# Optimization experiments

Hardware: AMD Instinct MI355X
Metric: run time of the kernel (lower is better)

## Reference

```python
import jax, jax.numpy as jnp
import numpy as np

HEADS = 16
DIM_HEAD = 64


def setup_inputs() -> dict:
    key = jax.random.key(0)
    k1, k2, k3 = jax.random.split(key, 3)
    b, n, dim = 8, 4096, 1024
    inner = HEADS * DIM_HEAD  # 1024
    x = jax.random.normal(k1, (b, n, dim), dtype=jnp.float32)
    # torch Linear stored transposed; here W_qkv is [in, out] so y = x @ W_qkv
    W_qkv = jax.random.normal(k2, (dim, 4 * inner), dtype=jnp.float32) * (dim ** -0.5)
    W_out = jax.random.normal(k3, (inner, dim), dtype=jnp.float32) * (inner ** -0.5)
    b_out = jnp.zeros((dim,), dtype=jnp.float32)
    return {"x": x, "W_qkv": W_qkv, "W_out": W_out, "b_out": b_out}


def reference(x, W_qkv, W_out, b_out):
    b, n, dim = x.shape
    h, d = HEADS, DIM_HEAD
    scale = d ** -0.5
    qkv = x @ W_qkv  # [b, n, 4*h*d]
    q, k, v, v2 = jnp.split(qkv, 4, axis=-1)
    # rearrange 'b n (h d) -> b h n d'
    to_heads = lambda t: t.reshape(b, n, h, d).transpose(0, 2, 1, 3)
    q, k, v, v2 = map(to_heads, (q, k, v, v2))
    # channel-wise attention: dots = q^T @ k over the sequence axis -> [b,h,d,d]
    dots = jnp.einsum('bhnd,bhne->bhde', q, k) * scale
    attn = jax.nn.softmax(dots, axis=-1)
    # v^T @ v2 -> [b,h,d,d]
    vv = jnp.einsum('bhnd,bhne->bhde', v, v2)
    out = jnp.einsum('bhde,bhef->bhdf', attn, vv)  # [b,h,d,d]
    # rearrange 'b h n d -> b n (h d)' with n == dim_head here
    out = out.transpose(0, 2, 1, 3).reshape(b, d, h * d)  # [b, dim_head, inner]
    return out @ W_out + b_out  # [b, dim_head, dim]
```

## Files before the change

### kernel.cpp

```cpp
#include <hip/hip_runtime.h>
#include <hip/hip_bf16.h>
#include <stdint.h>

typedef _Float16 f16;
typedef _Float16 f16x8 __attribute__((ext_vector_type(8)));
typedef float f32x4 __attribute__((ext_vector_type(4)));

#define AS1 __attribute__((address_space(1)))
#define AS3 __attribute__((address_space(3)))

__global__ __launch_bounds__(256) void tr_cvt_kernel(
    const float* __restrict__ src, f16* __restrict__ dst, int R, int C)
{
    __shared__ float tile[64][65];
    const int b = blockIdx.z;
    src += (size_t)b * R * C;
    dst += (size_t)b * R * C;
    const int c0 = blockIdx.x * 64;
    const int r0 = blockIdx.y * 64;
    const int t = threadIdx.x;
    {
        const int cc = (t & 15) * 4;
        const int rr = t >> 4;
#pragma unroll
        for (int p = 0; p < 4; ++p) {
            const int r = rr + p * 16;
            const float4 v = *(const float4*)(src + (size_t)(r0 + r) * C + c0 + cc);
            tile[r][cc + 0] = v.x; tile[r][cc + 1] = v.y;
            tile[r][cc + 2] = v.z; tile[r][cc + 3] = v.w;
        }
    }
    __syncthreads();
    {
        const int rq = (t & 15) * 4;
        const int cp = t >> 4;
#pragma unroll
        for (int p = 0; p < 4; ++p) {
            const int c = cp + p * 16;
            ushort4 o;
            f16 h0 = (f16)tile[rq + 0][c];
            f16 h1 = (f16)tile[rq + 1][c];
            f16 h2 = (f16)tile[rq + 2][c];
            f16 h3 = (f16)tile[rq + 3][c];
            o.x = __builtin_bit_cast(unsigned short, h0);
            o.y = __builtin_bit_cast(unsigned short, h1);
            o.z = __builtin_bit_cast(unsigned short, h2);
            o.w = __builtin_bit_cast(unsigned short, h3);
            *(ushort4*)(dst + (size_t)(c0 + c) * R + r0 + rq) = o;
        }
    }
}

__device__ __forceinline__ void stage256(
    const f16* __restrict__ src, int ld, char* ldsbase, int tid)
{
    const int lane = tid & 63;
    const int gch = ((lane & 7) ^ (lane >> 3)) * 8;
    const int rowl = tid >> 3;
    const int wbase = (tid >> 3) & ~7;
#pragma unroll
    for (int p = 0; p < 4; ++p) {
        const f16* s = src + (size_t)(p * 64 + rowl) * ld + gch;
        __builtin_amdgcn_global_load_lds(
            (const AS1 uint32_t*)s,
            (AS3 uint32_t*)(ldsbase + (p * 64 + wbase) * 128), 16, 0, 0);
    }
}

__device__ __forceinline__ void gemm256_core(
    const f16* __restrict__ A, const f16* __restrict__ Bt,
    int lda, int ldb, int nsteps,
    f16* As, f16* Bs, f32x4 (&acc)[8][4], int tid)
{
    const int lane = tid & 63, w = tid >> 6;
    const int wr = w >> 2, wc = w & 3;
    const int cl = lane & 15, kg = lane >> 4, b7 = lane & 7;

    stage256(A, lda, (char*)As, tid);
    stage256(Bt, ldb, (char*)Bs, tid);

#pragma unroll 1
    for (int t = 0; t < nsteps; ++t) {
        const int cur = t & 1;
        if (t + 1 < nsteps) {
            const int k0 = (t + 1) * 64;
            stage256(A + k0, lda, (char*)As + (cur ^ 1) * 32768, tid);
            stage256(Bt + k0, ldb, (char*)Bs + (cur ^ 1) * 32768, tid);
            asm volatile("s_waitcnt vmcnt(8)" ::: "memory");
        } else {
            asm volatile("s_waitcnt vmcnt(0)" ::: "memory");
        }
        __builtin_amdgcn_s_barrier();
        const f16* Ab = As + cur * 16384;
        const f16* Bb = Bs + cur * 16384;
#pragma unroll
        for (int kk = 0; kk < 2; ++kk) {
            const int ch = (kk * 4 + kg) ^ b7;
            f16x8 af[8], bf[4];
#pragma unroll
            for (int i = 0; i < 8; ++i)
                af[i] = *(const f16x8*)&Ab[(wr * 128 + i * 16 + cl) * 64 + ch * 8];
#pragma unroll
            for (int j = 0; j < 4; ++j)
                bf[j] = *(const f16x8*)&Bb[(wc * 64 + j * 16 + cl) * 64 + ch * 8];
#pragma unroll
            for (int i = 0; i < 8; ++i)
#pragma unroll
                for (int j = 0; j < 4; ++j)
                    acc[i][j] = __builtin_amdgcn_mfma_f32_16x16x32_f16(af[i], bf[j], acc[i][j], 0, 0, 0);
        }
        __builtin_amdgcn_s_barrier();
    }
}

__global__ __launch_bounds__(512, 2) void gemm_syk256(
    const f16* __restrict__ xT, f16* __restrict__ Gp)
{
    __shared__ f16 As[2 * 256 * 64];
    __shared__ f16 Bs[2 * 256 * 64];
    const int orig = blockIdx.x;
    const int l = (orig & 7) * 32 + (orig >> 3);
    const int tile = l & 15, b = (l >> 4) & 7, s = l >> 7;
    const int ti = tile >> 2, tj = tile & 3;

    const f16* base = xT + (size_t)b * (1024 * 4096) + (size_t)s * 2048;
    const f16* A  = base + (size_t)ti * 256 * 4096;
    const f16* Bt = base + (size_t)tj * 256 * 4096;

    f32x4 acc[8][4];
#pragma unroll
    for (int i = 0; i < 8; ++i)
#pragma unroll
        for (int j = 0; j < 4; ++j) acc[i][j] = f32x4{0.f, 0.f, 0.f, 0.f};

    gemm256_core(A, Bt, 4096, 4096, 32, As, Bs, acc, threadIdx.x);

    f16* out = Gp + ((size_t)s * 8 + b) * 1048576;
    const int lane = threadIdx.x & 63, w = threadIdx.x >> 6;
    const int wr = w >> 2, wc = w & 3;
    const int cl = lane & 15, rg = lane >> 4;
#pragma unroll
    for (int i = 0; i < 8; ++i)
#pragma unroll
        for (int j = 0; j < 4; ++j)
#pragma unroll
            for (int q = 0; q < 4; ++q) {
                const int row = ti * 256 + wr * 128 + i * 16 + rg * 4 + q;
                const int col = tj * 256 + wc * 64 + j * 16 + cl;
                out[(size_t)row * 1024 + col] = (f16)acc[i][j][q];
            }
}

__global__ __launch_bounds__(256) void reduce_sum(
    const f16* __restrict__ Gp, f16* __restrict__ G)
{
    const size_t i = ((size_t)blockIdx.x * 256 + threadIdx.x) * 8;
    const f16x8 a = *(const f16x8*)(Gp + i);
    const f16x8 c = *(const f16x8*)(Gp + 8388608 + i);
    f16x8 o;
#pragma unroll
    for (int j = 0; j < 8; ++j) o[j] = (f16)((float)a[j] + (float)c[j]);
    *(f16x8*)(G + i) = o;
}

__global__ __launch_bounds__(512, 2) void gemm_qv256(
    const f16* __restrict__ WqkvT, const f16* __restrict__ G,
    f16* __restrict__ UW2)
{
    __shared__ f16 As[2 * 256 * 64];
    __shared__ f16 Bs[2 * 256 * 64];
    const int orig = blockIdx.x;
    const int l = (orig & 7) * 32 + (orig >> 3);
    const int bx = l & 3, by = (l >> 2) & 7, b = l >> 5;
    const int arow = (by < 4) ? by * 256 : 2048 + (by - 4) * 256;

    const f16* A  = WqkvT + (size_t)arow * 1024;
    const f16* Bt = G + (size_t)b * 1048576 + (size_t)bx * 256 * 1024;

    f32x4 acc[8][4];
#pragma unroll
    for (int i = 0; i < 8; ++i)
#pragma unroll
        for (int j = 0; j < 4; ++j) acc[i][j] = f32x4{0.f, 0.f, 0.f, 0.f};

    gemm256_core(A, Bt, 1024, 1024, 16, As, Bs, acc, threadIdx.x);

    f16* C = UW2 + (size_t)b * 2097152;
    const int lane = threadIdx.x & 63, w = threadIdx.x >> 6;
    const int wr = w >> 2, wc = w & 3;
    const int cl = lane & 15, rg = lane >> 4;
#pragma unroll
    for (int i = 0; i < 8; ++i)
#pragma unroll
        for (int j = 0; j < 4; ++j) {
            const int cc = bx * 256 + wc * 64 + j * 16 + cl;
#pragma unroll
            for (int q = 0; q < 4; ++q) {
                const int rr = by * 256 + wr * 128 + i * 16 + rg * 4 + q;
                C[(size_t)rr * 1024 + cc] = (f16)acc[i][j][q];
            }
        }
}

__device__ __forceinline__ void gemm_body(
    const f16* __restrict__ A, const f16* __restrict__ Bt,
    int lda, int ldb, int K, f16* As, f16* Bs,
    f32x4 (&acc)[4][4], int tid)
{
    const int lane = tid & 63, w = tid >> 6;
    const int wr = w >> 1, wc = w & 1;
    const int lrow = lane >> 3;
    const int lcol = (lane & 7) * 8;
    for (int k0 = 0; k0 < K; k0 += 64) {
#pragma unroll
        for (int p = 0; p < 4; ++p) {
            const f16* sa = A + (size_t)(p * 32 + w * 8 + lrow) * lda + k0 + lcol;
            __builtin_amdgcn_global_load_lds(
                (const AS1 uint32_t*)sa,
                (AS3 uint32_t*)((char*)As + p * 4096 + w * 1024), 16, 0, 0);
            const f16* sb = Bt + (size_t)(p * 32 + w * 8 + lrow) * ldb + k0 + lcol;
            __builtin_amdgcn_global_load_lds(
                (const AS1 uint32_t*)sb,
                (AS3 uint32_t*)((char*)Bs + p * 4096 + w * 1024), 16, 0, 0);
        }
        __syncthreads();
#pragma unroll
        for (int kk = 0; kk < 2; ++kk) {
            f16x8 af[4], bfr[4];
#pragma unroll
            for (int i = 0; i < 4; ++i)
                af[i] = *(const f16x8*)&As[(wr * 64 + i * 16 + (lane & 15)) * 64 + kk * 32 + (lane >> 4) * 8];
#pragma unroll
            for (int j = 0; j < 4; ++j)
                bfr[j] = *(const f16x8*)&Bs[(wc * 64 + j * 16 + (lane & 15)) * 64 + kk * 32 + (lane >> 4) * 8];
#pragma unroll
            for (int i = 0; i < 4; ++i)
#pragma unroll
                for (int j = 0; j < 4; ++j)
                    acc[i][j] = __builtin_amdgcn_mfma_f32_16x16x32_f16(af[i], bfr[j], acc[i][j], 0, 0, 0);
        }
        __syncthreads();
    }
}

__global__ __launch_bounds__(256) void gemm_out(
    const f16* __restrict__ A, const f16* __restrict__ Bt,
    const float* __restrict__ bias, float* __restrict__ Cout)
{
    __shared__ f16 As[128 * 64];
    __shared__ f16 Bs[128 * 64];
    const int tn0 = blockIdx.x * 128;
    const int tm0 = blockIdx.y * 128;
    f32x4 acc[4][4];
#pragma unroll
    for (int i = 0; i < 4; ++i)
#pragma unroll
        for (int j = 0; j < 4; ++j) acc[i][j] = f32x4{0.f, 0.f, 0.f, 0.f};

    gemm_body(A + (size_t)tm0 * 1024, Bt + (size_t)tn0 * 1024,
              1024, 1024, 1024, As, Bs, acc, threadIdx.x);

    const int lane = threadIdx.x & 63, w = threadIdx.x >> 6;
    const int wr = w >> 1, wc = w & 1;
    const int cl = lane & 15, rg = lane >> 4;
#pragma unroll
    for (int i = 0; i < 4; ++i)
#pragma unroll
        for (int j = 0; j < 4; ++j) {
            const int cc = tn0 + wc * 64 + j * 16 + cl;
            const float bv = bias[cc];
#pragma unroll
            for (int q = 0; q < 4; ++q) {
                const int rr = tm0 + wr * 64 + i * 16 + rg * 4 + q;
                Cout[(size_t)rr * 1024 + cc] = acc[i][j][q] + bv;
            }
        }
}

__global__ __launch_bounds__(512) void attn_small(
    const f16* __restrict__ UW2, const f16* __restrict__ WqkvT,
    f16* __restrict__ O)
{
    __shared__ float dots[64][66];
    __shared__ float vv[64][66];
    const int h = blockIdx.x, b = blockIdx.y;
    const int tid = threadIdx.x, lane = tid & 63, w = tid >> 6;
    const int isVV = w >> 2;
    const int kq = w & 3;

    const f16* Arows = UW2 + (size_t)b * (2048 * 1024)
                           + (size_t)isVV * (1024 * 1024) + (size_t)h * 64 * 1024;
    const f16* Brows = WqkvT + (size_t)(isVV ? 3072 : 1024) * 1024 + (size_t)h * 64 * 1024;

    f32x4 acc[4][4];
#pragma unroll
    for (int i = 0; i < 4; ++i)
#pragma unroll
        for (int j = 0; j < 4; ++j) acc[i][j] = f32x4{0.f, 0.f, 0.f, 0.f};

    const int cl = lane & 15, kg = lane >> 4;
    for (int ks = 0; ks < 8; ++ks) {
        const int k0 = kq * 256 + ks * 32 + kg * 8;
        f16x8 af[4], bfr[4];
#pragma unroll
        for (int i = 0; i < 4; ++i)
            af[i] = *(const f16x8*)(Arows + (size_t)(i * 16 + cl) * 1024 + k0);
#pragma unroll
        for (int j = 0; j < 4; ++j)
            bfr[j] = *(const f16x8*)(Brows + (size_t)(j * 16 + cl) * 1024 + k0);
#pragma unroll
        for (int i = 0; i < 4; ++i)
#pragma unroll
            for (int j = 0; j < 4; ++j)
                acc[i][j] = __builtin_amdgcn_mfma_f32_16x16x32_f16(af[i], bfr[j], acc[i][j], 0, 0, 0);
    }

    float (*dst)[66] = isVV ? vv : dots;
#pragma unroll
    for (int r = 0; r < 4; ++r) {
        if (kq == r) {
            if (r == 0) {
#pragma unroll
                for (int i = 0; i < 4; ++i)
#pragma unroll
                    for (int j = 0; j < 4; ++j)
#pragma unroll
                        for (int q = 0; q < 4; ++q)
                            dst[i * 16 + kg * 4 + q][j * 16 + cl] = acc[i][j][q];
            } else {
#pragma unroll
                for (int i = 0; i < 4; ++i)
#pragma unroll
                    for (int j = 0; j < 4; ++j)
#pragma unroll
                        for (int q = 0; q < 4; ++q)
                            dst[i * 16 + kg * 4 + q][j * 16 + cl] += acc[i][j][q];
            }
        }
        __syncthreads();
    }

    if (tid < 64) {
        const int r = tid;
        float mx = -1e30f;
        for (int e = 0; e < 64; ++e) {
            const float v = dots[r][e] * 0.125f;
            dots[r][e] = v;
            mx = fmaxf(mx, v);
        }
        float s = 0.f;
        for (int e = 0; e < 64; ++e) {
            const float v = __expf(dots[r][e] - mx);
            dots[r][e] = v;
            s += v;
        }
        const float inv = 1.f / s;
        for (int e = 0; e < 64; ++e) dots[r][e] *= inv;
    }
    __syncthreads();

    {
        const int r = tid >> 3, f0 = (tid & 7) * 8;
        float o[8];
#pragma unroll
        for (int i = 0; i < 8; ++i) o[i] = 0.f;
        for (int e = 0; e < 64; ++e) {
            const float a = dots[r][e];
#pragma unroll
            for (int i = 0; i < 8; ++i) o[i] += a * vv[e][f0 + i];
        }
        f16* Od = O + (size_t)b * 64 * 1024 + (size_t)r * 1024 + h * 64 + f0;
#pragma unroll
        for (int i = 0; i < 8; ++i) Od[i] = (f16)o[i];
    }
}

extern "C" void kernel_launch(void* const* d_in, const int* in_sizes, int n_in,
                              void* d_out, int out_size, void* d_ws, size_t ws_size,
                              hipStream_t stream)
{
    const float* x    = (const float*)d_in[0];
    const float* Wqkv = (const float*)d_in[1];
    const float* Wout = (const float*)d_in[2];
    const float* bout = (const float*)d_in[3];

    char* ws = (char*)d_ws;
    f16* xT    = (f16*)(ws + 0);
    f16* WqkvT = (f16*)(ws + 67108864);
    f16* WoutT = (f16*)(ws + 75497472);
    f16* G     = (f16*)(ws + 77594624);
    f16* Gp    = (f16*)(ws + 94371840);
    f16* UW2   = (f16*)(ws + 94371840);
    f16* O     = (f16*)(ws + 127926272);

    tr_cvt_kernel<<<dim3(16, 64, 8), 256, 0, stream>>>(x, xT, 4096, 1024);
    tr_cvt_kernel<<<dim3(64, 16, 1), 256, 0, stream>>>(Wqkv, WqkvT, 1024, 4096);
    tr_cvt_kernel<<<dim3(16, 16, 1), 256, 0, stream>>>(Wout, WoutT, 1024, 1024);

    gemm_syk256<<<256, 512, 0, stream>>>(xT, Gp);
    reduce_sum<<<4096, 256, 0, stream>>>(Gp, G);
    gemm_qv256<<<256, 512, 0, stream>>>(WqkvT, G, UW2);
    attn_small<<<dim3(16, 8), 512, 0, stream>>>(UW2, WqkvT, O);
    gemm_out<<<dim3(8, 4), 256, 0, stream>>>(O, WoutT, bout, (float*)d_out);
}
```

Baseline: 201.6 us.

## Merge transpose-convert launches and fuse split-K reduction into GEMM via atomic counter

Combines the three fp32→fp16 transpose kernels into one launch with block-id dispatch, which also zeroes a counter array. The split-K reduction kernel is removed: each gemm_syk256 block writes its partial tile, fences, and bumps a per-tile atomic counter, and the second-arriving block adds the other partial and writes the final G tile. This saves two kernel launches and one full pass over the partial buffer. In exchange it adds fences and atomics and relies on cross-block memory visibility.

```diff
diff --git a/kernel.cpp b/kernel.cpp
--- a/kernel.cpp
+++ b/kernel.cpp
@@ -9,16 +9,36 @@
 #define AS1 __attribute__((address_space(1)))
 #define AS3 __attribute__((address_space(3)))
 
-__global__ __launch_bounds__(256) void tr_cvt_kernel(
-    const float* __restrict__ src, f16* __restrict__ dst, int R, int C)
+__global__ __launch_bounds__(256) void tr_cvt_all(
+    const float* __restrict__ x, const float* __restrict__ Wqkv,
+    const float* __restrict__ Wout,
+    f16* __restrict__ xT, f16* __restrict__ WqkvT, f16* __restrict__ WoutT,
+    unsigned* __restrict__ cnt)
 {
     __shared__ float tile[64][65];
-    const int b = blockIdx.z;
-    src += (size_t)b * R * C;
-    dst += (size_t)b * R * C;
-    const int c0 = blockIdx.x * 64;
-    const int r0 = blockIdx.y * 64;
+    const int id = blockIdx.x;
     const int t = threadIdx.x;
+    if (id == 0 && t < 128) cnt[t] = 0u;
+
+    const float* src; f16* dst; int R, C, c0, r0;
+    if (id < 8192) {
+        const int b = id >> 10, rem = id & 1023;
+        src = x + (size_t)b * 4096 * 1024;
+        dst = xT + (size_t)b * 4096 * 1024;
+        R = 4096; C = 1024;
+        c0 = (rem & 15) * 64; r0 = (rem >> 4) * 64;
+    } else if (id < 9216) {
+        const int rem = id - 8192;
+        src = Wqkv; dst = WqkvT;
+        R = 1024; C = 4096;
+        c0 = (rem & 63) * 64; r0 = (rem >> 6) * 64;
+    } else {
+        const int rem = id - 9216;
+        src = Wout; dst = WoutT;
+        R = 1024; C = 1024;
+        c0 = (rem & 15) * 64; r0 = (rem >> 4) * 64;
+    }
+
     {
         const int cc = (t & 15) * 4;
         const int rr = t >> 4;
@@ -114,10 +134,12 @@
 }
 
 __global__ __launch_bounds__(512, 2) void gemm_syk256(
-    const f16* __restrict__ xT, f16* __restrict__ Gp)
+    const f16* __restrict__ xT, f16* __restrict__ Gp,
+    f16* __restrict__ G, unsigned* __restrict__ cnt)
 {
     __shared__ f16 As[2 * 256 * 64];
     __shared__ f16 Bs[2 * 256 * 64];
+    __shared__ unsigned sold;
     const int orig = blockIdx.x;
     const int l = (orig & 7) * 32 + (orig >> 3);
     const int tile = l & 15, b = (l >> 4) & 7, s = l >> 7;
@@ -135,32 +157,44 @@
 
     gemm256_core(A, Bt, 4096, 4096, 32, As, Bs, acc, threadIdx.x);
 
-    f16* out = Gp + ((size_t)s * 8 + b) * 1048576;
-    const int lane = threadIdx.x & 63, w = threadIdx.x >> 6;
+    const int tid = threadIdx.x;
+    const int lane = tid & 63, w = tid >> 6;
     const int wr = w >> 2, wc = w & 3;
     const int cl = lane & 15, rg = lane >> 4;
+
+    f16* myGp = Gp + ((((size_t)s * 8 + b) * 16) + tile) * 65536;
 #pragma unroll
     for (int i = 0; i < 8; ++i)
 #pragma unroll
         for (int j = 0; j < 4; ++j)
 #pragma unroll
             for (int q = 0; q < 4; ++q) {
-                const int row = ti * 256 + wr * 128 + i * 16 + rg * 4 + q;
-                const int col = tj * 256 + wc * 64 + j * 16 + cl;
-                out[(size_t)row * 1024 + col] = (f16)acc[i][j][q];
+                const int lr = wr * 128 + i * 16 + rg * 4 + q;
+                const int lc = wc * 64 + j * 16 + cl;
+                myGp[lr * 256 + lc] = (f16)acc[i][j][q];
             }
-}
-
-__global__ __launch_bounds__(256) void reduce_sum(
-    const f16* __restrict__ Gp, f16* __restrict__ G)
-{
-    const size_t i = ((size_t)blockIdx.x * 256 + threadIdx.x) * 8;
-    const f16x8 a = *(const f16x8*)(Gp + i);
-    const f16x8 c = *(const f16x8*)(Gp + 8388608 + i);
-    f16x8 o;
-#pragma unroll
-    for (int j = 0; j < 8; ++j) o[j] = (f16)((float)a[j] + (float)c[j]);
-    *(f16x8*)(G + i) = o;
+
+    __threadfence();
+    __syncthreads();
+    if (tid == 0) sold = atomicAdd(&cnt[b * 16 + tile], 1u);
+    __syncthreads();
+    if ((sold & 1u) == 0u) return;
+
+    __threadfence();
+    const f16* other = Gp + ((((size_t)(s ^ 1) * 8 + b) * 16) + tile) * 65536;
+    f16* Gt = G + (size_t)b * 1048576 + (size_t)(ti * 256) * 1024 + tj * 256;
+#pragma unroll
+    for (int i = 0; i < 8; ++i)
+#pragma unroll
+        for (int j = 0; j < 4; ++j)
+#pragma unroll
+            for (int q = 0; q < 4; ++q) {
+                const int lr = wr * 128 + i * 16 + rg * 4 + q;
+                const int lc = wc * 64 + j * 16 + cl;
+                const float mine = (float)(f16)acc[i][j][q];
+                const float sum = mine + (float)other[lr * 256 + lc];
+                Gt[(size_t)lr * 1024 + lc] = (f16)sum;
+            }
 }
 
 __global__ __launch_bounds__(512, 2) void gemm_qv256(
@@ -385,20 +419,18 @@
     const float* bout = (const float*)d_in[3];
 
     char* ws = (char*)d_ws;
-    f16* xT    = (f16*)(ws + 0);
-    f16* WqkvT = (f16*)(ws + 67108864);
-    f16* WoutT = (f16*)(ws + 75497472);
-    f16* G     = (f16*)(ws + 77594624);
-    f16* Gp    = (f16*)(ws + 94371840);
-    f16* UW2   = (f16*)(ws + 94371840);
-    f16* O     = (f16*)(ws + 127926272);
-
-    tr_cvt_kernel<<<dim3(16, 64, 8), 256, 0, stream>>>(x, xT, 4096, 1024);
-    tr_cvt_kernel<<<dim3(64, 16, 1), 256, 0, stream>>>(Wqkv, WqkvT, 1024, 4096);
-    tr_cvt_kernel<<<dim3(16, 16, 1), 256, 0, stream>>>(Wout, WoutT, 1024, 1024);
-
-    gemm_syk256<<<256, 512, 0, stream>>>(xT, Gp);
-    reduce_sum<<<4096, 256, 0, stream>>>(Gp, G);
+    f16* xT       = (f16*)(ws + 0);
+    f16* WqkvT    = (f16*)(ws + 67108864);
+    f16* WoutT    = (f16*)(ws + 75497472);
+    f16* G        = (f16*)(ws + 77594624);
+    f16* Gp       = (f16*)(ws + 94371840);
+    f16* UW2      = (f16*)(ws + 94371840);
+    f16* O        = (f16*)(ws + 127926272);
+    unsigned* cnt = (unsigned*)(ws + 128974848);
+
+    tr_cvt_all<<<9472, 256, 0, stream>>>(x, Wqkv, Wout, xT, WqkvT, WoutT, cnt);
+
+    gemm_syk256<<<256, 512, 0, stream>>>(xT, Gp, G, cnt);
     gemm_qv256<<<256, 512, 0, stream>>>(WqkvT, G, UW2);
     attn_small<<<dim3(16, 8), 512, 0, stream>>>(UW2, WqkvT, O);
     gemm_out<<<dim3(8, 4), 256, 0, stream>>>(O, WoutT, bout, (float*)d_out);
```

Result: slower. 306.2 us (+51.9%).
